# Kernel optimization log

Measured on AMD Instinct MI355X. Metric: run time of the kernel, lower is better.

Reference implementation:

```python
import jax, jax.numpy as jnp
import numpy as np

B, L, D_IN, D_GATE, D_HID, D_STATE = 4, 8192, 512, 2048, 128, 512
EPS = 1e-5


def _layernorm(x, g, b):
    m = jnp.mean(x, axis=-1, keepdims=True)
    v = jnp.var(x, axis=-1, keepdims=True)
    return (x - m) * jax.lax.rsqrt(v + EPS) * g + b


def _dss(u, g, b, lam_re, lam_im, c_re, c_im, d):
    # u: [B, L, H]; diagonal state-space mixing along L via FFT conv
    seq_len = u.shape[-2]
    un = _layernorm(u, g, b)
    residual = un * d                                   # learned skip, [B,L,H]
    lam = -jnp.exp(lam_re) + 1j * jnp.exp(lam_im)       # [N] complex
    c = (c_re + 1j * c_im) * (jnp.exp(lam) - 1.0) / lam  # [H,N]
    t = jnp.arange(seq_len, dtype=jnp.float32)
    s = jnp.exp(t[:, None] * lam[None, :])              # [L,N] Vandermonde
    kern = jnp.einsum('hn,ln->lh', c, s).real           # [L,H]
    n_fft = 2 * seq_len
    uf = jnp.fft.rfft(un, n=n_fft, axis=-2)             # [B, n_fft/2+1, H]
    kf = jnp.fft.rfft(kern, n=n_fft, axis=0)            # [n_fft/2+1, H]
    y = jnp.fft.irfft(uf * kf, n=n_fft, axis=-2)[..., :seq_len, :]
    return y + residual


def setup_inputs() -> dict:
    key = jax.random.key(0)
    ks = jax.random.split(key, 16)
    f32 = jnp.float32
    return {
        'x': jax.random.normal(ks[0], (B, L, D_IN), f32),
        'norm_g': jnp.ones((D_IN,), f32),
        'norm_b': jnp.zeros((D_IN,), f32),
        'W_v': jax.random.normal(ks[1], (D_GATE, D_IN), f32) / np.sqrt(D_IN),
        'W_u': jax.random.normal(ks[2], (D_HID, D_IN), f32) / np.sqrt(D_IN),
        'W_uc': jax.random.normal(ks[3], (D_GATE, D_HID), f32) / np.sqrt(D_HID),
        'W_o': jax.random.normal(ks[4], (D_IN, D_GATE), f32) / np.sqrt(D_GATE),
        'b_o': jnp.zeros((D_IN,), f32),
        'dss_g': jnp.ones((D_HID,), f32),
        'dss_b': jnp.zeros((D_HID,), f32),
        'lam_re': jax.random.normal(ks[5], (D_STATE,), f32),
        'lam_im': jax.random.normal(ks[6], (D_STATE,), f32),
        'C_re': jax.random.normal(ks[7], (D_HID, D_STATE), f32) / np.sqrt(D_STATE),
        'C_im': jax.random.normal(ks[8], (D_HID, D_STATE), f32) / np.sqrt(D_STATE),
        'D_skip': jax.random.normal(ks[9], (D_HID,), f32),
    }


def reference(x, norm_g, norm_b, W_v, W_u, W_uc, W_o, b_o,
              dss_g, dss_b, lam_re, lam_im, C_re, C_im, D_skip):
    xn = _layernorm(x, norm_g, norm_b)
    v = jax.nn.gelu(jnp.einsum('blf,gf->blg', xn, W_v), approximate=False)  # [B,L,G]
    u = jax.nn.gelu(jnp.einsum('blf,hf->blh', xn, W_u), approximate=False)  # [B,L,H]
    y = _dss(u, dss_g, dss_b, lam_re, lam_im, C_re, C_im, D_skip)           # [B,L,H]
    uc = jnp.einsum('blh,gh->blg', y, W_uc)                                 # [B,L,G]
    o = jnp.einsum('blg,fg->blf', uc * v, W_o) + b_o                        # [B,L,F]
    return o + x
```

## Files before the change

kernel.cpp:

```cpp
#include <hip/hip_runtime.h>
#include <math.h>
#include <stdint.h>

typedef unsigned short u16;
typedef unsigned int   u32;
typedef short short8 __attribute__((ext_vector_type(8)));
typedef float v4f    __attribute__((ext_vector_type(4)));

#define DEVI static __device__ __forceinline__

struct __align__(8)  U2 { u32 x, y; };
struct __align__(16) U4 { u32 x, y, z, w; };

static const int BB = 4, LL = 8192;
static const int BL = BB * LL;

DEVI float bf2f(u16 u){ u32 v = ((u32)u) << 16; float f; __builtin_memcpy(&f, &v, 4); return f; }
DEVI u16  f2bf(float f){ u32 u; __builtin_memcpy(&u, &f, 4); return (u16)((u + 0x7fffu + ((u >> 16) & 1u)) >> 16); }

DEVI float geluf(float x){
  float z = fabsf(x) * 0.7071067811865475f;
  float t = __builtin_amdgcn_rcpf(1.0f + 0.3275911f * z);
  float p = t * (0.254829592f + t * (-0.284496736f + t * (1.421413741f +
            t * (-1.453152027f + t * 1.061405429f))));
  float e = __builtin_amdgcn_exp2f(z * z * -1.4426950408889634f);
  float er = 1.0f - p * e;
  float s = (x < 0.0f) ? -er : er;
  return 0.5f * x * (1.0f + s);
}

DEVI void ldsload16(const void* g, void* l){
  __builtin_amdgcn_global_load_lds(
      (const __attribute__((address_space(1))) u32*)(uintptr_t)g,
      (__attribute__((address_space(3)))  u32*)(u32)(uintptr_t)l,
      16, 0, 0);
}

__global__ __launch_bounds__(256) void k_cvt4(
    const float* __restrict__ s0, u16* __restrict__ d0, int n0,
    const float* __restrict__ s1, u16* __restrict__ d1, int n1,
    const float* __restrict__ s2, u16* __restrict__ d2, int n2,
    const float* __restrict__ s3, u16* __restrict__ d3, int n3){
  int i = blockIdx.x * 256 + threadIdx.x;
  if (i < n0){ d0[i] = f2bf(s0[i]); return; }
  i -= n0;
  if (i < n1){ d1[i] = f2bf(s1[i]); return; }
  i -= n1;
  if (i < n2){ d2[i] = f2bf(s2[i]); return; }
  i -= n2;
  if (i < n3){ d3[i] = f2bf(s3[i]); }
}

__global__ __launch_bounds__(256) void k_ln1(const float* __restrict__ x, const float* __restrict__ g,
                                             const float* __restrict__ b, u16* __restrict__ xn){
  int row = blockIdx.x, t = threadIdx.x;
  const float2* xr = (const float2*)(x + (int64_t)row * 512);
  float2 p = xr[t];
  float s = p.x + p.y, ss = p.x * p.x + p.y * p.y;
  for (int off = 32; off; off >>= 1){ s += __shfl_down(s, off); ss += __shfl_down(ss, off); }
  __shared__ float red[8];
  int w = t >> 6, lane = t & 63;
  if (!lane){ red[w] = s; red[4 + w] = ss; }
  __syncthreads();
  s  = red[0] + red[1] + red[2] + red[3];
  ss = red[4] + red[5] + red[6] + red[7];
  float m = s * (1.0f / 512.0f), var = ss * (1.0f / 512.0f) - m * m;
  float rs = rsqrtf(var + 1e-5f);
  float2 gv = ((const float2*)g)[t], bv = ((const float2*)b)[t];
  float r0 = (p.x - m) * rs * gv.x + bv.x;
  float r1 = (p.y - m) * rs * gv.y + bv.y;
  ((u32*)(xn + (int64_t)row * 512))[t] = (u32)f2bf(r0) | ((u32)f2bf(r1) << 16);
}

__global__ __launch_bounds__(256) void k_ln2(const u16* __restrict__ u, const float* __restrict__ g,
                                             const float* __restrict__ b, u16* __restrict__ un){
  int row = blockIdx.x * 4 + (threadIdx.x >> 6);
  int lane = threadIdx.x & 63;
  const u32* ur = (const u32*)(u + (int64_t)row * 128);
  u32 pv = ur[lane];
  float a = bf2f((u16)(pv & 0xffff)), c = bf2f((u16)(pv >> 16));
  float s = a + c, ss = a * a + c * c;
  for (int off = 32; off; off >>= 1){ s += __shfl_xor(s, off); ss += __shfl_xor(ss, off); }
  float m = s * (1.0f / 128.0f), var = ss * (1.0f / 128.0f) - m * m;
  float rs = rsqrtf(var + 1e-5f);
  float2 gv = ((const float2*)g)[lane], bv = ((const float2*)b)[lane];
  float r0 = (a - m) * rs * gv.x + bv.x;
  float r1 = (c - m) * rs * gv.y + bv.y;
  ((u32*)(un + (int64_t)row * 128))[lane] = (u32)f2bf(r0) | ((u32)f2bf(r1) << 16);
}

__global__ __launch_bounds__(256) void k_transpose(const u16* __restrict__ un, u16* __restrict__ unT){
  int bc = blockIdx.x >> 3, it = blockIdx.x & 7;
  int b = bc >> 4, cc = bc & 15;
  __shared__ __align__(16) u16 tile[64][128];
  const u16* src = un + ((int64_t)(b * 8192 + cc * 512 + it * 64)) * 128;
  int t = threadIdx.x;
  for (int p = 0; p < 4; p++){
    int id = p * 256 + t; int ri = id >> 4, seg = id & 15;
    *(U4*)&tile[ri][seg * 8] = *(const U4*)(src + (int64_t)ri * 128 + seg * 8);
  }
  __syncthreads();
  u16* dst = unT + ((int64_t)(bc * 128)) * 512 + it * 64;
  for (int p = 0; p < 4; p++){
    int id = p * 256 + t; int h = id >> 3, seg = id & 7;
    U4 pk; u16* pv = (u16*)&pk;
    for (int k2 = 0; k2 < 8; k2++) pv[k2] = tile[seg * 8 + k2][h];
    *(U4*)(dst + (int64_t)h * 512 + seg * 8) = pk;
  }
}

__global__ __launch_bounds__(512) void k_prep(const float* lam_re, const float* lam_im,
    const float* C_re, const float* C_im,
    u16* ZC, u16* PC, u16* VC, u16* ccat, float* cre, float* cim, float* zT){
  int n = blockIdx.x, t = threadIdx.x;
  float lr = -expf(lam_re[n]);
  float li =  expf(lam_im[n]);
  float mag = expf(lr * (float)t), ph = li * (float)t;
  float er = mag * cosf(ph), ei = mag * sinf(ph);
  ZC[(int64_t)n * 512 + (511 - t)]         = f2bf(er);
  ZC[(int64_t)(512 + n) * 512 + (511 - t)] = f2bf(ei);
  VC[(int64_t)t * 1024 + n]       = f2bf(er);
  VC[(int64_t)t * 1024 + 512 + n] = f2bf(-ei);
  float mag2 = expf(lr * (float)(t + 1)), ph2 = li * (float)(t + 1);
  PC[(int64_t)t * 1024 + n]       = f2bf(mag2 * cosf(ph2));
  PC[(int64_t)t * 1024 + 512 + n] = f2bf(-mag2 * sinf(ph2));
  if (t == 0){
    float m5 = expf(lr * 512.0f), p5 = li * 512.0f;
    zT[n] = m5 * cosf(p5); zT[512 + n] = m5 * sinf(p5);
  }
  if (t < 128){
    float e1m = expf(lr);
    float e1r = e1m * cosf(li), e1i = e1m * sinf(li);
    float nr = e1r - 1.0f, ni = e1i;
    float d2 = lr * lr + li * li;
    float qr = (nr * lr + ni * li) / d2, qi = (ni * lr - nr * li) / d2;
    float Cr = C_re[t * 512 + n], Ci = C_im[t * 512 + n];
    float vr = Cr * qr - Ci * qi, vi = Cr * qi + Ci * qr;
    cre[t * 512 + n] = vr; cim[t * 512 + n] = vi;
    ccat[(int64_t)t * 1024 + n] = f2bf(vr); ccat[(int64_t)t * 1024 + 512 + n] = f2bf(vi);
  }
}

__global__ __launch_bounds__(512) void k_rcat(const float* __restrict__ kern, u16* __restrict__ Rcat){
  int h = blockIdx.x >> 7, a = blockIdx.x & 127;
  int kcol = threadIdx.x;
  int d = 3 - (kcol >> 7);
  int delay = d * 128 + a - (kcol & 127);
  float val = (delay >= 0 && delay < 512) ? kern[delay * 128 + h] : 0.0f;
  Rcat[((int64_t)(h * 128 + a)) * 512 + kcol] = f2bf(val);
}

__global__ __launch_bounds__(256) void k_scan(const float* __restrict__ S, const float* __restrict__ cre,
    const float* __restrict__ cim, const float* __restrict__ zT, u16* __restrict__ WT){
  int tid = blockIdx.x * 256 + threadIdx.x;
  int n = tid & 511, bh = tid >> 9, b = bh >> 7, h = bh & 127;
  float cr = cre[h * 512 + n], ci = cim[h * 512 + n];
  float zr = zT[n], zi = zT[512 + n];
  float sR = 0.0f, sI = 0.0f;
  for (int cc = 0; cc < 16; cc++){
    int64_t m = (int64_t)(b * 16 + cc) * 128 + h;
    float wR = cr * sR - ci * sI, wI = cr * sI + ci * sR;
    WT[m * 1024 + n] = f2bf(wR);
    WT[m * 1024 + 512 + n] = f2bf(wI);
    float aR = S[m * 1024 + n], aI = S[m * 1024 + 512 + n];
    float nR = zr * sR - zi * sI + aR;
    sI = zr * sI + zi * sR + aI;
    sR = nR;
  }
}

__global__ __launch_bounds__(256) void k_assemble(const float* __restrict__ Yloc, const float* __restrict__ Ycross,
    const u16* __restrict__ un, const float* __restrict__ Dskip, u16* __restrict__ y){
  int64_t e = (int64_t)blockIdx.x * 256 + threadIdx.x;
  int h = (int)(e & 127); int64_t bl = e >> 7;
  int b = (int)(bl >> 13), l = (int)(bl & 8191);
  int cc = l >> 9, ii = l & 511, bc = b * 16 + cc;
  float val = Yloc[((int64_t)h * 512 + ii) * 64 + bc]
            + Ycross[(int64_t)ii * 8192 + (int64_t)bc * 128 + h]
            + bf2f(un[e]) * Dskip[h];
  y[e] = f2bf(val);
}

template<int EPI, bool TRI = false>
__global__ __launch_bounds__(256) void k_gemm(
    const u16* __restrict__ A, int64_t lda, int64_t aZ,
    const u16* __restrict__ B, int64_t ldb, int64_t bZ,
    void* Cp, int64_t ldc, int64_t cZ,
    int K, int Nvalid,
    const u16* aux1, const float* auxf1, const float* auxf2)
{
  __shared__ union __align__(16) SMU { u16 st[2][4096]; float ep[4][1088]; } sm;
  const int tid = threadIdx.x;
  const int lane = tid & 63, w = tid >> 6;
  const int wr = w >> 1, wc = w & 1, q = lane >> 4, c16 = lane & 15;
  const int sRow = lane >> 2, sSeg = lane & 3;
  const int z = blockIdx.z;

  int bx = blockIdx.x, by = blockIdx.y;
  if (!TRI && (gridDim.y & 7) == 0 && gridDim.x > 1){
    u32 idx = by * gridDim.x + bx;
    u32 xcd = idx & 7, s = idx >> 3;
    bx = s % gridDim.x;
    by = (s / gridDim.x) * 8 + xcd;
  }
  const int64_t m0 = (int64_t)by * 128;
  const int64_t n0 = (int64_t)bx * 128;

  const u16* Ab = A + (int64_t)z * aZ;
  const u16* Bp = B + (int64_t)z * bZ;
  int Keff = K;
  if (TRI){
    Ab += 384 - m0;
    Keff = (int)(m0 + 128);
  }

  v4f acc[4][4];
  #pragma unroll
  for (int i = 0; i < 4; i++)
    #pragma unroll
    for (int j = 0; j < 4; j++)
      acc[i][j] = (v4f)0.0f;

  for (int k0 = 0; k0 < Keff; k0 += 32){
    #pragma unroll
    for (int half = 0; half < 2; half++){
      int r0 = (half * 4 + w) * 16;
      int64_t arow = (TRI ? (int64_t)0 : m0) + r0 + sRow;
      ldsload16(Ab + arow * lda + k0 + sSeg * 8, &sm.st[0][r0 * 32]);
      int64_t brow = n0 + r0 + sRow;
      if (brow >= Nvalid) brow = Nvalid - 1;
      ldsload16(Bp + brow * ldb + k0 + sSeg * 8, &sm.st[1][r0 * 32]);
    }
    __syncthreads();
    short8 af[4], bfr[4];
    const u16* aB = &sm.st[0][(wr * 64 + c16) * 32 + q * 8];
    const u16* bB = &sm.st[1][(wc * 64 + c16) * 32 + q * 8];
    #pragma unroll
    for (int i = 0; i < 4; i++) af[i]  = *(const short8*)(aB + i * 512);
    #pragma unroll
    for (int j = 0; j < 4; j++) bfr[j] = *(const short8*)(bB + j * 512);
    #pragma unroll
    for (int i = 0; i < 4; i++)
      #pragma unroll
      for (int j = 0; j < 4; j++)
        acc[i][j] = __builtin_amdgcn_mfma_f32_16x16x32_bf16(af[i], bfr[j], acc[i][j], 0, 0, 0);
    __syncthreads();
  }

  if (EPI == 0){
    float* Cf = (float*)Cp + (int64_t)z * cZ;
    #pragma unroll
    for (int i = 0; i < 4; i++)
      #pragma unroll
      for (int j = 0; j < 4; j++){
        int64_t gr = m0 + wr * 64 + i * 16 + q * 4;
        int64_t gc = n0 + wc * 64 + j * 16 + c16;
        if (gc < Nvalid){
          #pragma unroll
          for (int r = 0; r < 4; r++)
            Cf[(gr + r) * ldc + gc] = acc[i][j][r];
        }
      }
    return;
  }

  u16* Cb = (u16*)Cp + (int64_t)z * cZ;
  float* ep = sm.ep[w];
  for (int i = 0; i < 4; i++){
    #pragma unroll
    for (int j = 0; j < 4; j++)
      #pragma unroll
      for (int r = 0; r < 4; r++){
        float vv = acc[i][j][r];
        if (EPI == 1) vv = geluf(vv);
        ep[(q * 4 + r) * 68 + j * 16 + c16] = vv;
      }
    #pragma unroll
    for (int p = 0; p < 4; p++){
      int id = p * 64 + lane;
      int row = id >> 4, cg = id & 15;
      float o0 = ep[row * 68 + cg * 4 + 0];
      float o1 = ep[row * 68 + cg * 4 + 1];
      float o2 = ep[row * 68 + cg * 4 + 2];
      float o3 = ep[row * 68 + cg * 4 + 3];
      int64_t gr = m0 + wr * 64 + i * 16 + row;
      int64_t gc = n0 + wc * 64 + cg * 4;
      if (gc < Nvalid){
        U2 outp;
        outp.x = (u32)f2bf(o0) | ((u32)f2bf(o1) << 16);
        outp.y = (u32)f2bf(o2) | ((u32)f2bf(o3) << 16);
        *(U2*)(Cb + gr * ldc + gc) = outp;
      }
    }
  }
}

#define FENCE __builtin_amdgcn_sched_barrier(0)
#define BARX  __builtin_amdgcn_s_barrier()

#define STAGE(SRC, LD, TBASE, SEL, KT)                                          \
  { const u16* _g = (SRC) + (int64_t)(KT) * 64 + (int64_t)((SEL) * 128 + wid * 8) * (LD); \
    u16* _lb = (TBASE) + ((SEL) * 128 + wid * 8) * 64;                          \
    ldsload16(_g, _lb);                                                         \
    ldsload16(_g + (int64_t)64 * (LD), _lb + 64 * 64);                          \
  }

#define MFMAQ(QM, QN, BQ)                                                       \
  __builtin_amdgcn_s_setprio(1);                                                \
  _Pragma("unroll")                                                             \
  for (int mi = 0; mi < 4; mi++)                                                \
    _Pragma("unroll")                                                           \
    for (int ni = 0; ni < 2; ni++){                                             \
      acc[(QM)*4+mi][(QN)*2+ni] = __builtin_amdgcn_mfma_f32_16x16x32_bf16(      \
          af[mi][0], BQ[ni][0], acc[(QM)*4+mi][(QN)*2+ni], 0, 0, 0);            \
      acc[(QM)*4+mi][(QN)*2+ni] = __builtin_amdgcn_mfma_f32_16x16x32_bf16(      \
          af[mi][1], BQ[ni][1], acc[(QM)*4+mi][(QN)*2+ni], 0, 0, 0);            \
    }                                                                           \
  __builtin_amdgcn_s_setprio(0);

#define DO_TILE(T, BUFC, BUFN)                                                  \
  {                                                                             \
    const char* Ac = (const char*)(BUFC);                                       \
    const char* Bc = (const char*)((BUFC) + 16384);                             \
    _Pragma("unroll")                                                           \
    for (int mi = 0; mi < 4; mi++){                                             \
      af[mi][0] = *(const short8*)(Ac + abase + mi * 2048 + kx0);               \
      af[mi][1] = *(const short8*)(Ac + abase + mi * 2048 + kx1);               \
    }                                                                           \
    _Pragma("unroll")                                                           \
    for (int ni = 0; ni < 2; ni++){                                             \
      bq0[ni][0] = *(const short8*)(Bc + bbase + ni * 2048 + kx0);              \
      bq0[ni][1] = *(const short8*)(Bc + bbase + ni * 2048 + kx1);              \
    }                                                                           \
    if ((T) + 1 < NT) STAGE(Bsrc, ldb, (BUFN) + 16384, 1, (T) + 1);             \
    FENCE; BARX; FENCE;                                                         \
    MFMAQ(0, 0, bq0);                                                           \
    FENCE; BARX; FENCE;                                                         \
    _Pragma("unroll")                                                           \
    for (int ni = 0; ni < 2; ni++){                                             \
      bq1[ni][0] = *(const short8*)(Bc + 16384 + bbase + ni * 2048 + kx0);      \
      bq1[ni][1] = *(const short8*)(Bc + 16384 + bbase + ni * 2048 + kx1);      \
    }                                                                           \
    if ((T) + 2 < NT) STAGE(Asrc, lda, (BUFC), 0, (T) + 2);                     \
    FENCE; BARX; FENCE;                                                         \
    MFMAQ(0, 1, bq1);                                                           \
    FENCE; BARX; FENCE;                                                         \
    _Pragma("unroll")                                                           \
    for (int mi = 0; mi < 4; mi++){                                             \
      af[mi][0] = *(const short8*)(Ac + 16384 + abase + mi * 2048 + kx0);       \
      af[mi][1] = *(const short8*)(Ac + 16384 + abase + mi * 2048 + kx1);       \
    }                                                                           \
    if ((T) + 2 < NT) STAGE(Bsrc, ldb, (BUFC) + 16384, 0, (T) + 2);             \
    FENCE; BARX; FENCE;                                                         \
    MFMAQ(1, 1, bq1);                                                           \
    FENCE; BARX; FENCE;                                                         \
    if ((T) + 2 < NT){                                                          \
      STAGE(Asrc, lda, (BUFC), 1, (T) + 2);                                     \
      asm volatile("s_waitcnt vmcnt(6)" ::: "memory");                          \
    } else {                                                                    \
      asm volatile("s_waitcnt vmcnt(0)" ::: "memory");                          \
    }                                                                           \
    FENCE; BARX; FENCE;                                                         \
    MFMAQ(1, 0, bq0);                                                           \
    FENCE; BARX; FENCE;                                                         \
  }

template<int EPI>
__global__ __launch_bounds__(512) void k_gemm256(
    const u16* __restrict__ A, int64_t lda,
    const u16* __restrict__ B, int64_t ldb,
    void* __restrict__ Cp, int64_t ldc, int K,
    const u16* __restrict__ aux1,
    const float* __restrict__ auxf1, const float* __restrict__ auxf2)
{
  extern __shared__ __align__(16) u16 smd[];
  const int tid = threadIdx.x, wid = tid >> 6, lane = tid & 63;
  const int wr = wid >> 2, wc = wid & 3, c16 = lane & 15;
  const int q4 = (lane >> 4) << 2;

  int bx = blockIdx.x, by = blockIdx.y;
  if ((gridDim.y & 7) == 0 && gridDim.x > 1){
    u32 idx = by * gridDim.x + bx;
    u32 xcd = idx & 7, s = idx >> 3;
    bx = s % gridDim.x;
    by = (s / gridDim.x) * 8 + xcd;
  }
  const int64_t m0 = (int64_t)by * 256;
  const int64_t n0 = (int64_t)bx * 256;
  const int NT = K >> 6;

  const int rowin = lane >> 3;
  const int colel = 8 * ((lane & 7) ^ rowin);
  const u16* Asrc = A + (m0 + rowin) * lda + colel;
  const u16* Bsrc = B + (n0 + rowin) * ldb + colel;

  const int kx0 = ((lane >> 4) << 4) ^ ((lane & 7) << 4);
  const int kx1 = kx0 ^ 64;
  const int abase = (wr * 64 + c16) * 128;
  const int bbase = (wc * 32 + c16) * 128;

  u16* buf0 = smd;
  u16* buf1 = smd + 32768;

  v4f acc[8][4];
  #pragma unroll
  for (int i = 0; i < 8; i++)
    #pragma unroll
    for (int j = 0; j < 4; j++) acc[i][j] = (v4f)0.0f;

  short8 af[4][2], bq0[2][2], bq1[2][2];

  STAGE(Asrc, lda, buf0,         0, 0);
  STAGE(Bsrc, ldb, buf0 + 16384, 0, 0);
  STAGE(Bsrc, ldb, buf0 + 16384, 1, 0);
  STAGE(Asrc, lda, buf0,         1, 0);
  if (NT > 1){
    STAGE(Asrc, lda, buf1,         0, 1);
    STAGE(Bsrc, ldb, buf1 + 16384, 0, 1);
    STAGE(Asrc, lda, buf1,         1, 1);
    asm volatile("s_waitcnt vmcnt(6)" ::: "memory");
  } else {
    asm volatile("s_waitcnt vmcnt(0)" ::: "memory");
  }
  FENCE; BARX; FENCE;

  for (int t = 0; t < NT; t += 2){
    DO_TILE(t,     buf0, buf1)
    DO_TILE(t + 1, buf1, buf0)
  }

  if (EPI == 0){
    float* C = (float*)Cp;
    #pragma unroll
    for (int qm = 0; qm < 2; qm++)
      #pragma unroll
      for (int mi = 0; mi < 4; mi++){
        int64_t gr = m0 + qm * 128 + wr * 64 + mi * 16 + q4;
        #pragma unroll
        for (int qn = 0; qn < 2; qn++)
          #pragma unroll
          for (int ni = 0; ni < 2; ni++){
            int64_t gc = n0 + qn * 128 + wc * 32 + ni * 16 + c16;
            v4f a = acc[qm * 4 + mi][qn * 2 + ni];
            float bo = auxf2[gc];
            #pragma unroll
            for (int r = 0; r < 4; r++)
              C[(gr + r) * ldc + gc] = a[r] + auxf1[(gr + r) * ldc + gc] + bo;
          }
      }
    return;
  }

  u16* Cb = (u16*)Cp;
  float* scr = (float*)smd + wid * 528;
  const int erow = lane >> 2, eseg = lane & 3;
  #pragma unroll
  for (int qm = 0; qm < 2; qm++)
    #pragma unroll
    for (int mi = 0; mi < 4; mi++)
      #pragma unroll
      for (int qn = 0; qn < 2; qn++){
        #pragma unroll
        for (int ni = 0; ni < 2; ni++){
          v4f a = acc[qm * 4 + mi][qn * 2 + ni];
          #pragma unroll
          for (int r = 0; r < 4; r++){
            float vv = a[r];
            if (EPI == 1) vv = geluf(vv);
            scr[(q4 + r) * 33 + ni * 16 + c16] = vv;
          }
        }
        float o[8];
        #pragma unroll
        for (int kq = 0; kq < 8; kq++) o[kq] = scr[erow * 33 + eseg * 8 + kq];
        int64_t gr = m0 + qm * 128 + wr * 64 + mi * 16 + erow;
        int64_t gc = n0 + qn * 128 + wc * 32 + eseg * 8;
        if (EPI == 2){
          U4 pv = *(const U4*)(aux1 + gr * ldc + gc);
          const u16* pp = (const u16*)&pv;
          #pragma unroll
          for (int kq = 0; kq < 8; kq++) o[kq] *= bf2f(pp[kq]);
        }
        U4 outp; u16* op = (u16*)&outp;
        #pragma unroll
        for (int kq = 0; kq < 8; kq++) op[kq] = f2bf(o[kq]);
        *(U4*)(Cb + gr * ldc + gc) = outp;
      }
}

extern "C" void kernel_launch(void* const* d_in, const int* in_sizes, int n_in,
                              void* d_out, int out_size, void* d_ws, size_t ws_size,
                              hipStream_t stream) {
  (void)in_sizes; (void)n_in; (void)out_size; (void)ws_size;
  const float* x      = (const float*)d_in[0];
  const float* norm_g = (const float*)d_in[1];
  const float* norm_b = (const float*)d_in[2];
  const float* W_v    = (const float*)d_in[3];
  const float* W_u    = (const float*)d_in[4];
  const float* W_uc   = (const float*)d_in[5];
  const float* W_o    = (const float*)d_in[6];
  const float* b_o    = (const float*)d_in[7];
  const float* dss_g  = (const float*)d_in[8];
  const float* dss_b  = (const float*)d_in[9];
  const float* lam_re = (const float*)d_in[10];
  const float* lam_im = (const float*)d_in[11];
  const float* C_re   = (const float*)d_in[12];
  const float* C_im   = (const float*)d_in[13];
  const float* D_skip = (const float*)d_in[14];

  char* ob = (char*)d_out;
  u16* xn    = (u16*)(ob);
  u16* Wv_b  = (u16*)(ob + 33554432ull);
  u16* Wu_b  = (u16*)(ob + 35651584ull);

  char* ws = (char*)d_ws;
  const size_t R1      = 134217728ull;
  const size_t OFF_UN  = R1 + 33554432ull;
  const size_t OFF_UNT = OFF_UN + 8388608ull;
  const size_t OFF_R2  = OFF_UNT + 8388608ull;
  const size_t OFF_TAB = OFF_R2 + 33554432ull;

  u16*  v     = (u16*)(ws + 0);
  u16*  u     = (u16*)(ws + R1);
  u16*  Rcat  = (u16*)(ws + R1);
  u16*  WT    = (u16*)(ws + R1 + 16777216ull);
  u16*  un    = (u16*)(ws + OFF_UN);
  u16*  unT   = (u16*)(ws + OFF_UNT);
  u16*  y     = (u16*)(ws + OFF_UNT);
  float* S    = (float*)(ws + OFF_R2);
  float* Ycross = (float*)(ws + OFF_R2);
  float* Yloc = (float*)(ws + OFF_R2 + 16777216ull);
  char* tp = ws + OFF_TAB;
  u16*  ZC   = (u16*)tp;            tp += 1048576;
  u16*  PC   = (u16*)tp;            tp += 1048576;
  u16*  VC   = (u16*)tp;            tp += 1048576;
  u16*  ccat = (u16*)tp;            tp += 262144;
  float* cre = (float*)tp;          tp += 262144;
  float* cim = (float*)tp;          tp += 262144;
  float* zT  = (float*)tp;          tp += 4096;
  float* kern= (float*)tp;          tp += 262144;
  u16*  Wo_b = (u16*)tp;            tp += 2097152;
  u16*  Wuc_b= (u16*)tp;            tp += 524288;

  k_cvt4<<<9472, 256, 0, stream>>>(W_v, Wv_b, 2048 * 512,
                                   W_u, Wu_b, 128 * 512,
                                   W_uc, Wuc_b, 2048 * 128,
                                   W_o, Wo_b, 512 * 2048);

  k_ln1<<<BL, 256, 0, stream>>>(x, norm_g, norm_b, xn);
  k_prep<<<512, 512, 0, stream>>>(lam_re, lam_im, C_re, C_im, ZC, PC, VC, ccat, cre, cim, zT);

  k_gemm256<1><<<dim3(8, 128), 512, 131072, stream>>>(xn, 512, Wv_b, 512, v, 2048, 512, nullptr, nullptr, nullptr);
  k_gemm<1><<<dim3(1, 256, 1), 256, 0, stream>>>(xn, 512, 0, Wu_b, 512, 0, u, 128, 0, 512, 128, nullptr, nullptr, nullptr);
  k_ln2<<<BL / 4, 256, 0, stream>>>(u, dss_g, dss_b, un);
  k_transpose<<<512, 256, 0, stream>>>(un, unT);

  k_gemm<0><<<dim3(1, 4, 1), 256, 0, stream>>>(VC, 1024, 0, ccat, 1024, 0, kern, 128, 0, 1024, 128, nullptr, nullptr, nullptr);
  k_rcat<<<16384, 512, 0, stream>>>(kern, Rcat);

  k_gemm<0><<<dim3(8, 64, 1), 256, 0, stream>>>(unT, 512, 0, ZC, 512, 0, S, 1024, 0, 512, 1024, nullptr, nullptr, nullptr);
  k_scan<<<1024, 256, 0, stream>>>(S, cre, cim, zT, WT);
  k_gemm<0><<<dim3(64, 4, 1), 256, 0, stream>>>(PC, 1024, 0, WT, 1024, 0, Ycross, 8192, 0, 1024, 8192, nullptr, nullptr, nullptr);
  k_gemm<0, true><<<dim3(1, 4, 128), 256, 0, stream>>>(
      Rcat, 512, 65536, unT, 65536, 512, Yloc, 64, 32768, 512, 64, nullptr, nullptr, nullptr);
  k_assemble<<<16384, 256, 0, stream>>>(Yloc, Ycross, un, D_skip, y);

  k_gemm256<2><<<dim3(8, 128), 512, 131072, stream>>>(y, 128, Wuc_b, 128, v, 2048, 128, v, nullptr, nullptr);
  k_gemm256<0><<<dim3(2, 128), 512, 131072, stream>>>(v, 2048, Wo_b, 2048, d_out, 512, 2048, nullptr, x, b_o);
}
```

Before: 590.1 us.

## Single-buffer gemm256 LDS pipeline for higher occupancy and add direct kern kernel

The 256x256 GEMM moves from a double-buffered LDS scheme (128 KB) to a single 64 KB buffer. Next-tile loads are staged into halves as soon as they have been consumed, and launch bounds are raised to allow more blocks per CU. The tiny kern GEMM is replaced by a simple dot-product kernel launched right after k_prep. The change trades prefetch depth for occupancy, and its correctness depends on the finer waitcnt and barrier ordering in the rewritten tile loop.

```diff
diff --git a/kernel.cpp b/kernel.cpp
--- a/kernel.cpp
+++ b/kernel.cpp
@@ -141,6 +141,25 @@
   }
 }
 
+__global__ __launch_bounds__(128) void k_kern(const u16* __restrict__ VC,
+                                              const u16* __restrict__ ccat,
+                                              float* __restrict__ kern){
+  __shared__ __align__(16) u16 vrow[1024];
+  int d = blockIdx.x, h = threadIdx.x;
+  *(U4*)&vrow[h * 8] = *(const U4*)(VC + (int64_t)d * 1024 + h * 8);
+  __syncthreads();
+  const u16* cr = ccat + (int64_t)h * 1024;
+  float s = 0.0f;
+  #pragma unroll 4
+  for (int k = 0; k < 1024; k += 8){
+    short8 a = *(const short8*)&vrow[k];
+    short8 b = *(const short8*)(cr + k);
+    #pragma unroll
+    for (int j = 0; j < 8; j++) s += bf2f((u16)a[j]) * bf2f((u16)b[j]);
+  }
+  kern[(int64_t)d * 128 + h] = s;
+}
+
 __global__ __launch_bounds__(512) void k_rcat(const float* __restrict__ kern, u16* __restrict__ Rcat){
   int h = blockIdx.x >> 7, a = blockIdx.x & 127;
   int kcol = threadIdx.x;
@@ -318,55 +337,65 @@
     }                                                                           \
   __builtin_amdgcn_s_setprio(0);
 
-#define DO_TILE(T, BUFC, BUFN)                                                  \
-  {                                                                             \
-    const char* Ac = (const char*)(BUFC);                                       \
-    const char* Bc = (const char*)((BUFC) + 16384);                             \
+#define DS_READ_A(OFF)                                                          \
     _Pragma("unroll")                                                           \
     for (int mi = 0; mi < 4; mi++){                                             \
-      af[mi][0] = *(const short8*)(Ac + abase + mi * 2048 + kx0);               \
-      af[mi][1] = *(const short8*)(Ac + abase + mi * 2048 + kx1);               \
-    }                                                                           \
+      af[mi][0] = *(const short8*)(Ac + (OFF) + abase + mi * 2048 + kx0);       \
+      af[mi][1] = *(const short8*)(Ac + (OFF) + abase + mi * 2048 + kx1);       \
+    }
+#define DS_READ_B(BQ, OFF)                                                      \
     _Pragma("unroll")                                                           \
     for (int ni = 0; ni < 2; ni++){                                             \
-      bq0[ni][0] = *(const short8*)(Bc + bbase + ni * 2048 + kx0);              \
-      bq0[ni][1] = *(const short8*)(Bc + bbase + ni * 2048 + kx1);              \
-    }                                                                           \
-    if ((T) + 1 < NT) STAGE(Bsrc, ldb, (BUFN) + 16384, 1, (T) + 1);             \
+      BQ[ni][0] = *(const short8*)(Bc + (OFF) + bbase + ni * 2048 + kx0);       \
+      BQ[ni][1] = *(const short8*)(Bc + (OFF) + bbase + ni * 2048 + kx1);       \
+    }
+
+#define DO_TILE_FULL(T)                                                         \
+  {                                                                             \
+    DS_READ_A(0) DS_READ_B(bq0, 0)                                              \
     FENCE; BARX; FENCE;                                                         \
     MFMAQ(0, 0, bq0);                                                           \
     FENCE; BARX; FENCE;                                                         \
-    _Pragma("unroll")                                                           \
-    for (int ni = 0; ni < 2; ni++){                                             \
-      bq1[ni][0] = *(const short8*)(Bc + 16384 + bbase + ni * 2048 + kx0);      \
-      bq1[ni][1] = *(const short8*)(Bc + 16384 + bbase + ni * 2048 + kx1);      \
-    }                                                                           \
-    if ((T) + 2 < NT) STAGE(Asrc, lda, (BUFC), 0, (T) + 2);                     \
+    DS_READ_B(bq1, 16384)                                                       \
+    STAGE(Asrc, lda, Abuf, 0, (T) + 1);                                         \
+    STAGE(Bsrc, ldb, Bbuf, 0, (T) + 1);                                         \
     FENCE; BARX; FENCE;                                                         \
     MFMAQ(0, 1, bq1);                                                           \
-    FENCE; BARX; FENCE;                                                         \
-    _Pragma("unroll")                                                           \
-    for (int mi = 0; mi < 4; mi++){                                             \
-      af[mi][0] = *(const short8*)(Ac + 16384 + abase + mi * 2048 + kx0);       \
-      af[mi][1] = *(const short8*)(Ac + 16384 + abase + mi * 2048 + kx1);       \
-    }                                                                           \
-    if ((T) + 2 < NT) STAGE(Bsrc, ldb, (BUFC) + 16384, 0, (T) + 2);             \
+    asm volatile("s_waitcnt vmcnt(4)" ::: "memory");                            \
+    FENCE; BARX; FENCE;                                                         \
+    DS_READ_A(16384)                                                            \
+    STAGE(Bsrc, ldb, Bbuf, 1, (T) + 1);                                         \
     FENCE; BARX; FENCE;                                                         \
     MFMAQ(1, 1, bq1);                                                           \
     FENCE; BARX; FENCE;                                                         \
-    if ((T) + 2 < NT){                                                          \
-      STAGE(Asrc, lda, (BUFC), 1, (T) + 2);                                     \
-      asm volatile("s_waitcnt vmcnt(6)" ::: "memory");                          \
-    } else {                                                                    \
-      asm volatile("s_waitcnt vmcnt(0)" ::: "memory");                          \
-    }                                                                           \
+    STAGE(Asrc, lda, Abuf, 1, (T) + 1);                                         \
+    asm volatile("s_waitcnt vmcnt(2)" ::: "memory");                            \
     FENCE; BARX; FENCE;                                                         \
     MFMAQ(1, 0, bq0);                                                           \
     FENCE; BARX; FENCE;                                                         \
   }
 
+#define DO_TILE_LAST                                                            \
+  {                                                                             \
+    DS_READ_A(0) DS_READ_B(bq0, 0)                                              \
+    FENCE; BARX; FENCE;                                                         \
+    MFMAQ(0, 0, bq0);                                                           \
+    FENCE; BARX; FENCE;                                                         \
+    DS_READ_B(bq1, 16384)                                                       \
+    FENCE; BARX; FENCE;                                                         \
+    MFMAQ(0, 1, bq1);                                                           \
+    asm volatile("s_waitcnt vmcnt(0)" ::: "memory");                            \
+    FENCE; BARX; FENCE;                                                         \
+    DS_READ_A(16384)                                                            \
+    FENCE; BARX; FENCE;                                                         \
+    MFMAQ(1, 1, bq1);                                                           \
+    FENCE; BARX; FENCE;                                                         \
+    MFMAQ(1, 0, bq0);                                                           \
+    FENCE; BARX; FENCE;                                                         \
+  }
+
 template<int EPI>
-__global__ __launch_bounds__(512) void k_gemm256(
+__global__ __launch_bounds__(512, 4) void k_gemm256(
     const u16* __restrict__ A, int64_t lda,
     const u16* __restrict__ B, int64_t ldb,
     void* __restrict__ Cp, int64_t ldc, int K,
@@ -399,8 +428,10 @@
   const int abase = (wr * 64 + c16) * 128;
   const int bbase = (wc * 32 + c16) * 128;
 
-  u16* buf0 = smd;
-  u16* buf1 = smd + 32768;
+  u16* Abuf = smd;
+  u16* Bbuf = smd + 16384;
+  const char* Ac = (const char*)smd;
+  const char* Bc = (const char*)smd + 32768;
 
   v4f acc[8][4];
   #pragma unroll
@@ -410,24 +441,16 @@
 
   short8 af[4][2], bq0[2][2], bq1[2][2];
 
-  STAGE(Asrc, lda, buf0,         0, 0);
-  STAGE(Bsrc, ldb, buf0 + 16384, 0, 0);
-  STAGE(Bsrc, ldb, buf0 + 16384, 1, 0);
-  STAGE(Asrc, lda, buf0,         1, 0);
-  if (NT > 1){
-    STAGE(Asrc, lda, buf1,         0, 1);
-    STAGE(Bsrc, ldb, buf1 + 16384, 0, 1);
-    STAGE(Asrc, lda, buf1,         1, 1);
-    asm volatile("s_waitcnt vmcnt(6)" ::: "memory");
-  } else {
-    asm volatile("s_waitcnt vmcnt(0)" ::: "memory");
-  }
+  STAGE(Asrc, lda, Abuf, 0, 0);
+  STAGE(Bsrc, ldb, Bbuf, 0, 0);
+  STAGE(Bsrc, ldb, Bbuf, 1, 0);
+  STAGE(Asrc, lda, Abuf, 1, 0);
+  asm volatile("s_waitcnt vmcnt(2)" ::: "memory");
   FENCE; BARX; FENCE;
 
-  for (int t = 0; t < NT; t += 2){
-    DO_TILE(t,     buf0, buf1)
-    DO_TILE(t + 1, buf1, buf0)
-  }
+  for (int t = 0; t < NT - 1; ++t)
+    DO_TILE_FULL(t)
+  DO_TILE_LAST
 
   if (EPI == 0){
     float* C = (float*)Cp;
@@ -549,13 +572,13 @@
 
   k_ln1<<<BL, 256, 0, stream>>>(x, norm_g, norm_b, xn);
   k_prep<<<512, 512, 0, stream>>>(lam_re, lam_im, C_re, C_im, ZC, PC, VC, ccat, cre, cim, zT);
-
-  k_gemm256<1><<<dim3(8, 128), 512, 131072, stream>>>(xn, 512, Wv_b, 512, v, 2048, 512, nullptr, nullptr, nullptr);
+  k_kern<<<512, 128, 0, stream>>>(VC, ccat, kern);
+
+  k_gemm256<1><<<dim3(8, 128), 512, 65536, stream>>>(xn, 512, Wv_b, 512, v, 2048, 512, nullptr, nullptr, nullptr);
   k_gemm<1><<<dim3(1, 256, 1), 256, 0, stream>>>(xn, 512, 0, Wu_b, 512, 0, u, 128, 0, 512, 128, nullptr, nullptr, nullptr);
   k_ln2<<<BL / 4, 256, 0, stream>>>(u, dss_g, dss_b, un);
   k_transpose<<<512, 256, 0, stream>>>(un, unT);
 
-  k_gemm<0><<<dim3(1, 4, 1), 256, 0, stream>>>(VC, 1024, 0, ccat, 1024, 0, kern, 128, 0, 1024, 128, nullptr, nullptr, nullptr);
   k_rcat<<<16384, 512, 0, stream>>>(kern, Rcat);
 
   k_gemm<0><<<dim3(8, 64, 1), 256, 0, stream>>>(unT, 512, 0, ZC, 512, 0, S, 1024, 0, 512, 1024, nullptr, nullptr, nullptr);
@@ -565,6 +588,6 @@
       Rcat, 512, 65536, unT, 65536, 512, Yloc, 64, 32768, 512, 64, nullptr, nullptr, nullptr);
   k_assemble<<<16384, 256, 0, stream>>>(Yloc, Ycross, un, D_skip, y);
 
-  k_gemm256<2><<<dim3(8, 128), 512, 131072, stream>>>(y, 128, Wuc_b, 128, v, 2048, 128, v, nullptr, nullptr);
-  k_gemm256<0><<<dim3(2, 128), 512, 131072, stream>>>(v, 2048, Wo_b, 2048, d_out, 512, 2048, nullptr, x, b_o);
-}
+  k_gemm256<2><<<dim3(8, 128), 512, 65536, stream>>>(y, 128, Wuc_b, 128, v, 2048, 128, v, nullptr, nullptr);
+  k_gemm256<0><<<dim3(2, 128), 512, 65536, stream>>>(v, 2048, Wo_b, 2048, d_out, 512, 2048, nullptr, x, b_o);
+}
```

Result: slower. 2.122 ms (+259.6%).
